# Optimization experiments

Hardware: AMD Instinct MI355X
Metric: run time of the kernel (lower is better)

## Reference

```python
import jax, jax.numpy as jnp
import numpy as np

N = 100000   # nodes
E = 1600000  # edges
G = 512      # graphs in batch
F_IN = 30
H = 128
EPS = 1e-5   # BatchNorm1d default eps


def setup_inputs() -> dict:
    key = jax.random.key(0)
    ks = jax.random.split(key, 16)
    x = jax.random.normal(ks[0], (N, F_IN), dtype=jnp.float32)
    edge_index = jax.random.randint(ks[1], (2, E), 0, N, dtype=jnp.int64)
    batch = jnp.sort(jax.random.randint(ks[2], (N,), 0, G, dtype=jnp.int64))
    d = {"x": x, "edge_index": edge_index, "batch": batch}
    dims = [(F_IN, H), (H, H), (H, H)]
    for i, (din, dout) in enumerate(dims):
        d[f"W{i}"] = jax.random.normal(ks[3 + i], (din, dout), dtype=jnp.float32) * (1.0 / np.sqrt(din))
        d[f"b{i}"] = jnp.zeros((dout,), dtype=jnp.float32)
        d[f"g{i}"] = jnp.ones((dout,), dtype=jnp.float32)   # BN gamma
        d[f"bt{i}"] = jnp.zeros((dout,), dtype=jnp.float32)  # BN beta
    d["HW1"] = jax.random.normal(ks[9], (H, 64), dtype=jnp.float32) * (1.0 / np.sqrt(H))
    d["Hb1"] = jnp.zeros((64,), dtype=jnp.float32)
    d["HW2"] = jax.random.normal(ks[10], (64, 1), dtype=jnp.float32) * 0.125
    d["Hb2"] = jnp.zeros((1,), dtype=jnp.float32)
    return d


def _bn(x, gamma, beta):
    # training-mode BatchNorm1d over node dim, biased variance (as torch uses for normalization)
    mu = jnp.mean(x, axis=0)
    var = jnp.mean(jnp.square(x - mu), axis=0)
    return (x - mu) * jax.lax.rsqrt(var + EPS) * gamma + beta


def reference(x, edge_index, batch, W0, b0, g0, bt0, W1, b1, g1, bt1, W2, b2, g2, bt2, HW1, Hb1, HW2, Hb2):
    # GCNConv: add self-loops, symmetric D^{-1/2}(A+I)D^{-1/2} normalization
    loop = jnp.arange(N, dtype=edge_index.dtype)
    src = jnp.concatenate([edge_index[0], loop])  # [E+N]
    dst = jnp.concatenate([edge_index[1], loop])
    deg = jax.ops.segment_sum(jnp.ones(src.shape, jnp.float32), dst, num_segments=N)
    dinv = jax.lax.rsqrt(jnp.maximum(deg, 1.0))  # deg >= 1 due to self-loops
    norm = (dinv[src] * dinv[dst])[:, None]      # [E+N, 1]

    for W, b, g, bt in ((W0, b0, g0, bt0), (W1, b1, g1, bt1), (W2, b2, g2, bt2)):
        h = x @ W                                           # [N, H]
        agg = jax.ops.segment_sum(h[src] * norm, dst, num_segments=N) + b
        x = jnp.maximum(_bn(agg, g, bt), 0.0)               # BN + ReLU (dropout = identity here)

    # global_mean_pool over graph ids
    counts = jax.ops.segment_sum(jnp.ones((N,), jnp.float32), batch, num_segments=G)
    pooled = jax.ops.segment_sum(x, batch, num_segments=G) / jnp.maximum(counts, 1.0)[:, None]

    h = jnp.maximum(pooled @ HW1 + Hb1, 0.0)
    return (h @ HW2 + Hb2).squeeze(-1)  # [G]
```

## Files before the change

### kernel.cpp

```cpp
#include <hip/hip_runtime.h>

#define BN_EPS 1e-5f
#define BSH 8

typedef __attribute__((ext_vector_type(8))) short bf16x8;
typedef __attribute__((ext_vector_type(4))) float f32x4;

__device__ inline float bfhi(unsigned int v) { return __uint_as_float(v & 0xFFFF0000u); }
__device__ inline float bflo(unsigned int v) { return __uint_as_float(v << 16); }
__device__ inline unsigned short f2bf(float f) {
  unsigned int u = __float_as_uint(f);
  u += 0x7FFFu + ((u >> 16) & 1u);
  return (unsigned short)(u >> 16);
}
__device__ inline unsigned int pack2bf(float lo, float hi) {
  return (unsigned int)f2bf(lo) | ((unsigned int)f2bf(hi) << 16);
}

__global__ void k_bucket(const int* __restrict__ src, const int* __restrict__ dst,
                         int* __restrict__ gcur, uint2* __restrict__ sedge,
                         int NB, int CAP, int E) {
  __shared__ int lh[512], rb[512];
  int tid = threadIdx.x;
  for (int i = tid; i < NB; i += 256) lh[i] = 0;
  __syncthreads();
  int base = blockIdx.x * 8192;
  int lim = min(8192, E - base);
  for (int i = tid; i < lim; i += 256)
    atomicAdd(&lh[dst[base + i] >> BSH], 1);
  __syncthreads();
  for (int i = tid; i < NB; i += 256) {
    int c = lh[i];
    rb[i] = c ? atomicAdd(&gcur[i], c) : 0;
    lh[i] = 0;
  }
  __syncthreads();
  for (int i = tid; i < lim; i += 256) {
    int d = dst[base + i];
    int s = src[base + i];
    int b = d >> BSH;
    int pos = rb[b] + atomicAdd(&lh[b], 1);
    if (pos < CAP) {
      uint2 v; v.x = (unsigned int)s; v.y = (unsigned int)d;
      sedge[(size_t)b * CAP + pos] = v;
    }
  }
}

__global__ void k_csr1(const uint2* __restrict__ sedge, const int* __restrict__ gcur,
                       int* __restrict__ startv, int* __restrict__ cnt,
                       float* __restrict__ dinv, int CAP, int n) {
  int b = blockIdx.x, tid = threadIdx.x;
  __shared__ int h[256], sc[256];
  h[tid] = 0;
  __syncthreads();
  int cb = gcur[b]; if (cb > CAP) cb = CAP;
  const uint2* sd = sedge + (size_t)b * CAP;
  for (int i = tid; i < cb; i += 256) atomicAdd(&h[sd[i].y & 255], 1);
  __syncthreads();
  int v = h[tid];
  sc[tid] = v;
  __syncthreads();
  for (int o = 1; o < 256; o <<= 1) {
    int t = (tid >= o) ? sc[tid - o] : 0;
    __syncthreads();
    sc[tid] += t;
    __syncthreads();
  }
  int gd = (b << BSH) + tid;
  if (gd < n) {
    startv[gd] = b * CAP + (sc[tid] - v);
    cnt[gd] = v;
    dinv[gd] = rsqrtf((float)v + 1.0f);
  }
}

__global__ void k_csr2(const uint2* __restrict__ sedge, const int* __restrict__ gcur,
                       const int* __restrict__ startv, const float* __restrict__ dinv,
                       unsigned int* __restrict__ elist, int CAP, int n) {
  int b = blockIdx.x, tid = threadIdx.x;
  __shared__ int cur[256];
  int gd = (b << BSH) + tid;
  cur[tid] = (gd < n) ? startv[gd] : 0;
  __syncthreads();
  int cb = gcur[b]; if (cb > CAP) cb = CAP;
  const uint2* sd = sedge + (size_t)b * CAP;
  for (int i = tid; i < cb; i += 256) {
    uint2 e = sd[i];
    int pos = atomicAdd(&cur[e.y & 255], 1);
    unsigned int u = (unsigned int)(dinv[e.x] * 32767.0f + 0.5f);
    elist[pos] = e.x | (u << 17);
  }
}

__global__ void k_cvtall(const float* __restrict__ x, const float* __restrict__ W0,
                         const float* __restrict__ W1, const float* __restrict__ W2,
                         unsigned short* __restrict__ xb, unsigned short* __restrict__ Wt0,
                         unsigned short* __restrict__ Wt1, unsigned short* __restrict__ Wt2,
                         int n) {
  int t = blockIdx.x * blockDim.x + threadIdx.x;
  if (t < 4096) {
    int nn = t >> 5, k = t & 31;
    Wt0[t] = f2bf(k < 30 ? W0[k * 128 + nn] : 0.f);
  } else if (t < 20480) {
    int i = t - 4096; int nn = i >> 7, k = i & 127;
    Wt1[i] = f2bf(W1[k * 128 + nn]);
  } else if (t < 36864) {
    int i = t - 20480; int nn = i >> 7, k = i & 127;
    Wt2[i] = f2bf(W2[k * 128 + nn]);
  } else {
    int i = t - 36864;
    if (i < n * 32) {
      int row = i >> 5, c = i & 31;
      xb[i] = f2bf(c < 30 ? x[row * 30 + c] : 0.f);
    }
  }
}

__global__ void k_gemm_mfma(const unsigned short* __restrict__ A,
                            const unsigned short* __restrict__ Wt,
                            const float* __restrict__ scsh, int doBN,
                            unsigned short* __restrict__ C, int n, int Kp) {
  __shared__ float ssc[128], ssh[128];
  if (doBN) {
    if (threadIdx.x < 128) {
      ssc[threadIdx.x] = scsh[threadIdx.x];
      ssh[threadIdx.x] = scsh[128 + threadIdx.x];
    }
    __syncthreads();
  }
  int wave = threadIdx.x >> 6;
  int lane = threadIdx.x & 63;
  int m0 = blockIdx.x * 128 + wave * 32;
  if (m0 >= n) return;
  int lm = lane & 15;
  int lq = lane >> 4;

  f32x4 acc[2][8] = {};
  const unsigned short* Arow0 = A + (size_t)(m0 + lm) * Kp + lq * 8;
  const unsigned short* Arow1 = Arow0 + (size_t)16 * Kp;
  const unsigned short* Bbase = Wt + (size_t)lm * Kp + lq * 8;

  for (int k0 = 0; k0 < Kp; k0 += 32) {
    uint4 ra0 = *(const uint4*)(Arow0 + k0);
    uint4 ra1 = *(const uint4*)(Arow1 + k0);
    bf16x8 a0, a1;
    if (doBN) {
      int cb = k0 + lq * 8;
      unsigned int w0 = pack2bf(fmaxf(fmaf(bflo(ra0.x), ssc[cb+0], ssh[cb+0]), 0.f),
                                fmaxf(fmaf(bfhi(ra0.x), ssc[cb+1], ssh[cb+1]), 0.f));
      unsigned int w1 = pack2bf(fmaxf(fmaf(bflo(ra0.y), ssc[cb+2], ssh[cb+2]), 0.f),
                                fmaxf(fmaf(bfhi(ra0.y), ssc[cb+3], ssh[cb+3]), 0.f));
      unsigned int w2 = pack2bf(fmaxf(fmaf(bflo(ra0.z), ssc[cb+4], ssh[cb+4]), 0.f),
                                fmaxf(fmaf(bfhi(ra0.z), ssc[cb+5], ssh[cb+5]), 0.f));
      unsigned int w3 = pack2bf(fmaxf(fmaf(bflo(ra0.w), ssc[cb+6], ssh[cb+6]), 0.f),
                                fmaxf(fmaf(bfhi(ra0.w), ssc[cb+7], ssh[cb+7]), 0.f));
      uint4 pa0 = make_uint4(w0, w1, w2, w3);
      a0 = *(bf16x8*)&pa0;
      unsigned int y0 = pack2bf(fmaxf(fmaf(bflo(ra1.x), ssc[cb+0], ssh[cb+0]), 0.f),
                                fmaxf(fmaf(bfhi(ra1.x), ssc[cb+1], ssh[cb+1]), 0.f));
      unsigned int y1 = pack2bf(fmaxf(fmaf(bflo(ra1.y), ssc[cb+2], ssh[cb+2]), 0.f),
                                fmaxf(fmaf(bfhi(ra1.y), ssc[cb+3], ssh[cb+3]), 0.f));
      unsigned int y2 = pack2bf(fmaxf(fmaf(bflo(ra1.z), ssc[cb+4], ssh[cb+4]), 0.f),
                                fmaxf(fmaf(bfhi(ra1.z), ssc[cb+5], ssh[cb+5]), 0.f));
      unsigned int y3 = pack2bf(fmaxf(fmaf(bflo(ra1.w), ssc[cb+6], ssh[cb+6]), 0.f),
                                fmaxf(fmaf(bfhi(ra1.w), ssc[cb+7], ssh[cb+7]), 0.f));
      uint4 pa1 = make_uint4(y0, y1, y2, y3);
      a1 = *(bf16x8*)&pa1;
    } else {
      a0 = *(bf16x8*)&ra0;
      a1 = *(bf16x8*)&ra1;
    }
#pragma unroll
    for (int t = 0; t < 8; ++t) {
      bf16x8 b = *(const bf16x8*)(Bbase + (size_t)t * 16 * Kp + k0);
      acc[0][t] = __builtin_amdgcn_mfma_f32_16x16x32_bf16(a0, b, acc[0][t], 0, 0, 0);
      acc[1][t] = __builtin_amdgcn_mfma_f32_16x16x32_bf16(a1, b, acc[1][t], 0, 0, 0);
    }
  }
#pragma unroll
  for (int h = 0; h < 2; ++h) {
    int rbase = m0 + h * 16 + lq * 4;
#pragma unroll
    for (int t = 0; t < 8; ++t) {
      int col = t * 16 + lm;
#pragma unroll
      for (int r = 0; r < 4; ++r) {
        int row = rbase + r;
        if (row < n) C[(size_t)row * 128 + col] = f2bf(acc[h][t][r]);
      }
    }
  }
}

__global__ void k_gather(const unsigned int* __restrict__ elist, const int* __restrict__ start,
                         const int* __restrict__ cnt, const float* __restrict__ dinv,
                         const uint4* __restrict__ h4,
                         const float* __restrict__ bias, unsigned int* __restrict__ agg,
                         float* __restrict__ bnsumP, int n) {
  int lane = threadIdx.x & 63;
  int wv   = threadIdx.x >> 6;
  int grp  = lane >> 4;
  int c8   = lane & 15;
  int row  = blockIdx.x * 4 + wv;
  bool active = row < n;

  float acc[8];
  float di = 0.f, dq = 0.f;
  int len = 0;
  const unsigned int* ep = elist;

  if (active) {
    di = dinv[row];
    dq = di * (1.0f / 32767.0f);
    len = cnt[row];
    ep = elist + start[row];
  }

  {
    float selfw = (grp == 0 && active) ? di * di : 0.f;
    float4 b0 = make_float4(0.f, 0.f, 0.f, 0.f), b1 = b0;
    if (grp == 0 && active) {
      b0 = ((const float4*)bias)[c8 * 2];
      b1 = ((const float4*)bias)[c8 * 2 + 1];
    }
    uint4 hv = active ? h4[(size_t)row * 16 + c8] : make_uint4(0, 0, 0, 0);
    acc[0] = fmaf(bflo(hv.x), selfw, b0.x);
    acc[1] = fmaf(bfhi(hv.x), selfw, b0.y);
    acc[2] = fmaf(bflo(hv.y), selfw, b0.z);
    acc[3] = fmaf(bfhi(hv.y), selfw, b0.w);
    acc[4] = fmaf(bflo(hv.z), selfw, b1.x);
    acc[5] = fmaf(bfhi(hv.z), selfw, b1.y);
    acc[6] = fmaf(bflo(hv.w), selfw, b1.z);
    acc[7] = fmaf(bfhi(hv.w), selfw, b1.w);
  }

  int j = 0;
  for (; j + 16 <= len; j += 16) {
    unsigned int e0 = ep[j + grp];
    unsigned int e1 = ep[j + 4 + grp];
    unsigned int e2 = ep[j + 8 + grp];
    unsigned int e3 = ep[j + 12 + grp];
    uint4 v0 = h4[(size_t)(e0 & 0x1FFFFu) * 16 + c8];
    uint4 v1 = h4[(size_t)(e1 & 0x1FFFFu) * 16 + c8];
    uint4 v2 = h4[(size_t)(e2 & 0x1FFFFu) * 16 + c8];
    uint4 v3 = h4[(size_t)(e3 & 0x1FFFFu) * 16 + c8];
    float w0 = (float)(e0 >> 17) * dq;
    float w1 = (float)(e1 >> 17) * dq;
    float w2 = (float)(e2 >> 17) * dq;
    float w3 = (float)(e3 >> 17) * dq;
    acc[0] = fmaf(bflo(v0.x), w0, acc[0]); acc[1] = fmaf(bfhi(v0.x), w0, acc[1]);
    acc[2] = fmaf(bflo(v0.y), w0, acc[2]); acc[3] = fmaf(bfhi(v0.y), w0, acc[3]);
    acc[4] = fmaf(bflo(v0.z), w0, acc[4]); acc[5] = fmaf(bfhi(v0.z), w0, acc[5]);
    acc[6] = fmaf(bflo(v0.w), w0, acc[6]); acc[7] = fmaf(bfhi(v0.w), w0, acc[7]);
    acc[0] = fmaf(bflo(v1.x), w1, acc[0]); acc[1] = fmaf(bfhi(v1.x), w1, acc[1]);
    acc[2] = fmaf(bflo(v1.y), w1, acc[2]); acc[3] = fmaf(bfhi(v1.y), w1, acc[3]);
    acc[4] = fmaf(bflo(v1.z), w1, acc[4]); acc[5] = fmaf(bfhi(v1.z), w1, acc[5]);
    acc[6] = fmaf(bflo(v1.w), w1, acc[6]); acc[7] = fmaf(bfhi(v1.w), w1, acc[7]);
    acc[0] = fmaf(bflo(v2.x), w2, acc[0]); acc[1] = fmaf(bfhi(v2.x), w2, acc[1]);
    acc[2] = fmaf(bflo(v2.y), w2, acc[2]); acc[3] = fmaf(bfhi(v2.y), w2, acc[3]);
    acc[4] = fmaf(bflo(v2.z), w2, acc[4]); acc[5] = fmaf(bfhi(v2.z), w2, acc[5]);
    acc[6] = fmaf(bflo(v2.w), w2, acc[6]); acc[7] = fmaf(bfhi(v2.w), w2, acc[7]);
    acc[0] = fmaf(bflo(v3.x), w3, acc[0]); acc[1] = fmaf(bfhi(v3.x), w3, acc[1]);
    acc[2] = fmaf(bflo(v3.y), w3, acc[2]); acc[3] = fmaf(bfhi(v3.y), w3, acc[3]);
    acc[4] = fmaf(bflo(v3.z), w3, acc[4]); acc[5] = fmaf(bfhi(v3.z), w3, acc[5]);
    acc[6] = fmaf(bflo(v3.w), w3, acc[6]); acc[7] = fmaf(bfhi(v3.w), w3, acc[7]);
  }
  for (; j < len; j += 4) {
    int jj = j + grp;
    unsigned int e = (jj < len) ? ep[jj] : 0u;
    uint4 v = h4[(size_t)(e & 0x1FFFFu) * 16 + c8];
    float w = (float)(e >> 17) * dq;
    acc[0] = fmaf(bflo(v.x), w, acc[0]); acc[1] = fmaf(bfhi(v.x), w, acc[1]);
    acc[2] = fmaf(bflo(v.y), w, acc[2]); acc[3] = fmaf(bfhi(v.y), w, acc[3]);
    acc[4] = fmaf(bflo(v.z), w, acc[4]); acc[5] = fmaf(bfhi(v.z), w, acc[5]);
    acc[6] = fmaf(bflo(v.w), w, acc[6]); acc[7] = fmaf(bfhi(v.w), w, acc[7]);
  }

#pragma unroll
  for (int k = 0; k < 8; ++k) {
    acc[k] += __shfl_xor(acc[k], 16);
    acc[k] += __shfl_xor(acc[k], 32);
  }

  __shared__ float sm[2][4][128];
  if (lane < 16) {
    if (active) {
      uint4 o;
      o.x = pack2bf(acc[0], acc[1]);
      o.y = pack2bf(acc[2], acc[3]);
      o.z = pack2bf(acc[4], acc[5]);
      o.w = pack2bf(acc[6], acc[7]);
      ((uint4*)agg)[(size_t)row * 16 + c8] = o;
    }
#pragma unroll
    for (int k = 0; k < 8; ++k) {
      float a = acc[k];
      sm[0][wv][c8 * 8 + k] = a;
      sm[1][wv][c8 * 8 + k] = a * a;
    }
  }
  __syncthreads();
  int tid = threadIdx.x;
  int slab = (blockIdx.x & 63) * 256;
  if (tid < 128) {
    float s = sm[0][0][tid] + sm[0][1][tid] + sm[0][2][tid] + sm[0][3][tid];
    atomicAdd(&bnsumP[slab + tid], s);
  } else {
    int c = tid - 128;
    float s = sm[1][0][c] + sm[1][1][c] + sm[1][2][c] + sm[1][3][c];
    atomicAdd(&bnsumP[slab + 128 + c], s);
  }
}

__global__ void k_bnfinal(const float* __restrict__ bnsumP, const float* __restrict__ gamma,
                          const float* __restrict__ beta, float* __restrict__ scsh, int n) {
  int c = threadIdx.x;
  float s = 0.f, s2 = 0.f;
  for (int k = 0; k < 64; ++k) {
    s  += bnsumP[k * 256 + c];
    s2 += bnsumP[k * 256 + 128 + c];
  }
  float invn = 1.0f / (float)n;
  float mu  = s * invn;
  float ex2 = s2 * invn;
  float var = fmaxf(ex2 - mu * mu, 0.f);
  float sc = gamma[c] * rsqrtf(var + BN_EPS);
  scsh[c] = sc;
  scsh[128 + c] = fmaf(-mu, sc, beta[c]);
}

__global__ void k_poolhead(const unsigned int* __restrict__ aggd, const float* __restrict__ scsh,
                           const int* __restrict__ batch, const float* __restrict__ HW1,
                           const float* __restrict__ Hb1, const float* __restrict__ HW2,
                           const float* __restrict__ Hb2, float* __restrict__ out, int n) {
  int g = blockIdx.x, t = threadIdx.x;
  int lo = 0, hi = n;
  while (lo < hi) { int mid = (lo + hi) >> 1; if (batch[mid] < g) lo = mid + 1; else hi = mid; }
  int s = lo;
  lo = 0; hi = n;
  int g1 = g + 1;
  while (lo < hi) { int mid = (lo + hi) >> 1; if (batch[mid] < g1) lo = mid + 1; else hi = mid; }
  int e = lo;

  float sc0 = scsh[2 * t], sc1 = scsh[2 * t + 1];
  float sh0 = scsh[128 + 2 * t], sh1 = scsh[128 + 2 * t + 1];
  float a0 = 0.f, a1 = 0.f;
  for (int i = s; i < e; ++i) {
    unsigned int u = aggd[(size_t)i * 64 + t];
    a0 += fmaxf(fmaf(bflo(u), sc0, sh0), 0.f);
    a1 += fmaxf(fmaf(bfhi(u), sc1, sh1), 0.f);
  }
  float inv = 1.0f / fmaxf((float)(e - s), 1.f);
  __shared__ float p[128];
  p[2 * t] = a0 * inv;
  p[2 * t + 1] = a1 * inv;
  __syncthreads();
  float acc = Hb1[t];
  for (int k = 0; k < 128; ++k) acc = fmaf(p[k], HW1[k * 64 + t], acc);
  float v = fmaxf(acc, 0.f) * HW2[t];
  for (int off = 32; off > 0; off >>= 1) v += __shfl_down(v, off);
  if (t == 0) out[g] = v + Hb2[0];
}

extern "C" void kernel_launch(void* const* d_in, const int* in_sizes, int n_in,
                              void* d_out, int out_size, void* d_ws, size_t ws_size,
                              hipStream_t stream) {
  const int F_IN = 30, H = 128;
  const float* x   = (const float*)d_in[0];
  const int* eidx  = (const int*)d_in[1];
  const int* batch = (const int*)d_in[2];
  const int N = in_sizes[0] / F_IN;
  const int E = in_sizes[1] / 2;
  const int G = out_size;
  const int* srcp = eidx;
  const int* dstp = eidx + E;
  const float* HW1 = (const float*)d_in[15];
  const float* Hb1 = (const float*)d_in[16];
  const float* HW2 = (const float*)d_in[17];
  const float* Hb2 = (const float*)d_in[18];
  float* outp = (float*)d_out;

  const int Npad = (N + 127) & ~127;
  size_t nh = (size_t)Npad * H;
  const int NB = (N + 255) >> BSH;
  const int CAP = ((E / NB) * 3) / 2 + 128;
  const int NBpad = (NB + 63) & ~63;

  unsigned short* bufH = (unsigned short*)d_ws;
  unsigned short* xbf  = bufH + nh;
  unsigned short* bufX = xbf + nh;
  float* dinv = (float*)(bufX + nh);
  int*   cnt    = (int*)(dinv + N);
  int*   startv = cnt + N;
  int*   gcur   = startv + N;
  float* bnsumP = (float*)(gcur + NBpad);
  float* scsh   = bnsumP + 3 * 64 * 256;
  unsigned short* Wt0 = (unsigned short*)(scsh + 256);
  unsigned short* Wt1 = Wt0 + 128 * 32;
  unsigned short* Wt2 = Wt1 + 128 * 128;
  unsigned int* elist = (unsigned int*)(Wt2 + 128 * 128 + 64);
  uint2* sedge = (uint2*)bufX;

  hipMemsetAsync(gcur, 0, ((size_t)NBpad + 3 * 64 * 256) * sizeof(int), stream);

  k_bucket<<<(E + 8191) / 8192, 256, 0, stream>>>(srcp, dstp, gcur, sedge, NB, CAP, E);
  k_csr1<<<NB, 256, 0, stream>>>(sedge, gcur, startv, cnt, dinv, CAP, N);
  k_csr2<<<NB, 256, 0, stream>>>(sedge, gcur, startv, dinv, elist, CAP, N);

  k_cvtall<<<(36864 + N * 32 + 255) / 256, 256, 0, stream>>>(
      x, (const float*)d_in[3], (const float*)d_in[7], (const float*)d_in[11],
      xbf, Wt0, Wt1, Wt2, N);

  const unsigned short* Wts[3] = {Wt0, Wt1, Wt2};
  for (int l = 0; l < 3; ++l) {
    const float* b  = (const float*)d_in[4 + l * 4];
    const float* gm = (const float*)d_in[5 + l * 4];
    const float* bt = (const float*)d_in[6 + l * 4];
    int Kp = (l == 0) ? 32 : 128;
    const unsigned short* Ain = (l == 0) ? xbf : bufX;
    float* bnslab = bnsumP + (size_t)l * 64 * 256;

    k_gemm_mfma<<<Npad / 128, 256, 0, stream>>>(Ain, Wts[l], scsh, l > 0, bufH, N, Kp);
    k_gather<<<(N + 3) / 4, 256, 0, stream>>>(elist, startv, cnt, dinv,
                                              (const uint4*)bufH, b,
                                              (unsigned int*)bufX, bnslab, N);
    k_bnfinal<<<1, 128, 0, stream>>>(bnslab, gm, bt, scsh, N);
  }

  k_poolhead<<<G, 64, 0, stream>>>((const unsigned int*)bufX, scsh, batch,
                                   HW1, Hb1, HW2, Hb2, outp, N);
}
```

Baseline: 523.2 us.

## Aggregate layer-0 before the GEMM, fuse BN stats into GEMM, parallelize pooling

```diff
diff --git a/kernel.cpp b/kernel.cpp
--- a/kernel.cpp
+++ b/kernel.cpp
@@ -117,10 +117,67 @@
   }
 }
 
+__global__ void k_gather0(const unsigned int* __restrict__ elist, const int* __restrict__ start,
+                          const int* __restrict__ cnt, const float* __restrict__ dinv,
+                          const uint4* __restrict__ x4,
+                          unsigned int* __restrict__ G0, int n) {
+  int lane = threadIdx.x & 63;
+  int wv   = threadIdx.x >> 6;
+  int grp  = lane >> 2;
+  int q4   = lane & 3;
+  int row  = blockIdx.x * 4 + wv;
+  bool active = row < n;
+
+  float acc[8];
+  float di = 0.f, dq = 0.f;
+  int len = 0;
+  const unsigned int* ep = elist;
+  if (active) {
+    di = dinv[row];
+    dq = di * (1.0f / 32767.0f);
+    len = cnt[row];
+    ep = elist + start[row];
+  }
+  {
+    float selfw = (grp == 0 && active) ? di * di : 0.f;
+    uint4 hv = (grp == 0 && active) ? x4[(size_t)row * 4 + q4] : make_uint4(0, 0, 0, 0);
+    acc[0] = bflo(hv.x) * selfw; acc[1] = bfhi(hv.x) * selfw;
+    acc[2] = bflo(hv.y) * selfw; acc[3] = bfhi(hv.y) * selfw;
+    acc[4] = bflo(hv.z) * selfw; acc[5] = bfhi(hv.z) * selfw;
+    acc[6] = bflo(hv.w) * selfw; acc[7] = bfhi(hv.w) * selfw;
+  }
+  for (int j = 0; j < len; j += 16) {
+    int jj = j + grp;
+    unsigned int e = (jj < len) ? ep[jj] : 0u;
+    uint4 v = x4[(size_t)(e & 0x1FFFFu) * 4 + q4];
+    float w = (float)(e >> 17) * dq;
+    acc[0] = fmaf(bflo(v.x), w, acc[0]); acc[1] = fmaf(bfhi(v.x), w, acc[1]);
+    acc[2] = fmaf(bflo(v.y), w, acc[2]); acc[3] = fmaf(bfhi(v.y), w, acc[3]);
+    acc[4] = fmaf(bflo(v.z), w, acc[4]); acc[5] = fmaf(bfhi(v.z), w, acc[5]);
+    acc[6] = fmaf(bflo(v.w), w, acc[6]); acc[7] = fmaf(bfhi(v.w), w, acc[7]);
+  }
+#pragma unroll
+  for (int k = 0; k < 8; ++k) {
+    acc[k] += __shfl_xor(acc[k], 4);
+    acc[k] += __shfl_xor(acc[k], 8);
+    acc[k] += __shfl_xor(acc[k], 16);
+    acc[k] += __shfl_xor(acc[k], 32);
+  }
+  if (grp == 0 && active) {
+    uint4 o;
+    o.x = pack2bf(acc[0], acc[1]);
+    o.y = pack2bf(acc[2], acc[3]);
+    o.z = pack2bf(acc[4], acc[5]);
+    o.w = pack2bf(acc[6], acc[7]);
+    ((uint4*)G0)[(size_t)row * 4 + q4] = o;
+  }
+}
+
 __global__ void k_gemm_mfma(const unsigned short* __restrict__ A,
                             const unsigned short* __restrict__ Wt,
                             const float* __restrict__ scsh, int doBN,
-                            unsigned short* __restrict__ C, int n, int Kp) {
+                            const float* __restrict__ bias, float* __restrict__ bnslab,
+                            int doStats, unsigned short* __restrict__ C, int n, int Kp) {
   __shared__ float ssc[128], ssh[128];
   if (doBN) {
     if (threadIdx.x < 128) {
@@ -132,7 +189,6 @@
   int wave = threadIdx.x >> 6;
   int lane = threadIdx.x & 63;
   int m0 = blockIdx.x * 128 + wave * 32;
-  if (m0 >= n) return;
   int lm = lane & 15;
   int lq = lane >> 4;
 
@@ -178,18 +234,49 @@
       acc[1][t] = __builtin_amdgcn_mfma_f32_16x16x32_bf16(a1, b, acc[1][t], 0, 0, 0);
     }
   }
+
 #pragma unroll
   for (int h = 0; h < 2; ++h) {
     int rbase = m0 + h * 16 + lq * 4;
 #pragma unroll
     for (int t = 0; t < 8; ++t) {
       int col = t * 16 + lm;
+      float bv = doStats ? bias[col] : 0.f;
 #pragma unroll
       for (int r = 0; r < 4; ++r) {
         int row = rbase + r;
-        if (row < n) C[(size_t)row * 128 + col] = f2bf(acc[h][t][r]);
+        if (row < n) C[(size_t)row * 128 + col] = f2bf(acc[h][t][r] + bv);
       }
     }
+  }
+
+  if (doStats) {
+    __shared__ float sms[4][256];
+#pragma unroll
+    for (int t = 0; t < 8; ++t) {
+      int col = t * 16 + lm;
+      float bv = bias[col];
+      float s = 0.f, s2 = 0.f;
+#pragma unroll
+      for (int h = 0; h < 2; ++h) {
+        int rbase = m0 + h * 16 + lq * 4;
+#pragma unroll
+        for (int r = 0; r < 4; ++r) {
+          if (rbase + r < n) {
+            float v = acc[h][t][r] + bv;
+            s += v; s2 = fmaf(v, v, s2);
+          }
+        }
+      }
+      s  += __shfl_xor(s, 16);  s  += __shfl_xor(s, 32);
+      s2 += __shfl_xor(s2, 16); s2 += __shfl_xor(s2, 32);
+      if (lq == 0) { sms[wave][col] = s; sms[wave][128 + col] = s2; }
+    }
+    __syncthreads();
+    int tid = threadIdx.x;
+    int slab = (blockIdx.x & 63) * 256;
+    float tot = sms[0][tid] + sms[1][tid] + sms[2][tid] + sms[3][tid];
+    atomicAdd(&bnslab[slab + tid], tot);
   }
 }
 
@@ -236,19 +323,13 @@
   }
 
   int j = 0;
-  for (; j + 16 <= len; j += 16) {
+  for (; j + 8 <= len; j += 8) {
     unsigned int e0 = ep[j + grp];
     unsigned int e1 = ep[j + 4 + grp];
-    unsigned int e2 = ep[j + 8 + grp];
-    unsigned int e3 = ep[j + 12 + grp];
     uint4 v0 = h4[(size_t)(e0 & 0x1FFFFu) * 16 + c8];
     uint4 v1 = h4[(size_t)(e1 & 0x1FFFFu) * 16 + c8];
-    uint4 v2 = h4[(size_t)(e2 & 0x1FFFFu) * 16 + c8];
-    uint4 v3 = h4[(size_t)(e3 & 0x1FFFFu) * 16 + c8];
     float w0 = (float)(e0 >> 17) * dq;
     float w1 = (float)(e1 >> 17) * dq;
-    float w2 = (float)(e2 >> 17) * dq;
-    float w3 = (float)(e3 >> 17) * dq;
     acc[0] = fmaf(bflo(v0.x), w0, acc[0]); acc[1] = fmaf(bfhi(v0.x), w0, acc[1]);
     acc[2] = fmaf(bflo(v0.y), w0, acc[2]); acc[3] = fmaf(bfhi(v0.y), w0, acc[3]);
     acc[4] = fmaf(bflo(v0.z), w0, acc[4]); acc[5] = fmaf(bfhi(v0.z), w0, acc[5]);
@@ -257,14 +338,6 @@
     acc[2] = fmaf(bflo(v1.y), w1, acc[2]); acc[3] = fmaf(bfhi(v1.y), w1, acc[3]);
     acc[4] = fmaf(bflo(v1.z), w1, acc[4]); acc[5] = fmaf(bfhi(v1.z), w1, acc[5]);
     acc[6] = fmaf(bflo(v1.w), w1, acc[6]); acc[7] = fmaf(bfhi(v1.w), w1, acc[7]);
-    acc[0] = fmaf(bflo(v2.x), w2, acc[0]); acc[1] = fmaf(bfhi(v2.x), w2, acc[1]);
-    acc[2] = fmaf(bflo(v2.y), w2, acc[2]); acc[3] = fmaf(bfhi(v2.y), w2, acc[3]);
-    acc[4] = fmaf(bflo(v2.z), w2, acc[4]); acc[5] = fmaf(bfhi(v2.z), w2, acc[5]);
-    acc[6] = fmaf(bflo(v2.w), w2, acc[6]); acc[7] = fmaf(bfhi(v2.w), w2, acc[7]);
-    acc[0] = fmaf(bflo(v3.x), w3, acc[0]); acc[1] = fmaf(bfhi(v3.x), w3, acc[1]);
-    acc[2] = fmaf(bflo(v3.y), w3, acc[2]); acc[3] = fmaf(bfhi(v3.y), w3, acc[3]);
-    acc[4] = fmaf(bflo(v3.z), w3, acc[4]); acc[5] = fmaf(bfhi(v3.z), w3, acc[5]);
-    acc[6] = fmaf(bflo(v3.w), w3, acc[6]); acc[7] = fmaf(bfhi(v3.w), w3, acc[7]);
   }
   for (; j < len; j += 4) {
     int jj = j + grp;
@@ -334,7 +407,8 @@
                            const int* __restrict__ batch, const float* __restrict__ HW1,
                            const float* __restrict__ Hb1, const float* __restrict__ HW2,
                            const float* __restrict__ Hb2, float* __restrict__ out, int n) {
-  int g = blockIdx.x, t = threadIdx.x;
+  int g = blockIdx.x;
+  int wv = threadIdx.x >> 6, t = threadIdx.x & 63;
   int lo = 0, hi = n;
   while (lo < hi) { int mid = (lo + hi) >> 1; if (batch[mid] < g) lo = mid + 1; else hi = mid; }
   int s = lo;
@@ -346,21 +420,27 @@
   float sc0 = scsh[2 * t], sc1 = scsh[2 * t + 1];
   float sh0 = scsh[128 + 2 * t], sh1 = scsh[128 + 2 * t + 1];
   float a0 = 0.f, a1 = 0.f;
-  for (int i = s; i < e; ++i) {
+  for (int i = s + wv; i < e; i += 4) {
     unsigned int u = aggd[(size_t)i * 64 + t];
     a0 += fmaxf(fmaf(bflo(u), sc0, sh0), 0.f);
     a1 += fmaxf(fmaf(bfhi(u), sc1, sh1), 0.f);
   }
-  float inv = 1.0f / fmaxf((float)(e - s), 1.f);
-  __shared__ float p[128];
-  p[2 * t] = a0 * inv;
-  p[2 * t + 1] = a1 * inv;
-  __syncthreads();
-  float acc = Hb1[t];
-  for (int k = 0; k < 128; ++k) acc = fmaf(p[k], HW1[k * 64 + t], acc);
-  float v = fmaxf(acc, 0.f) * HW2[t];
-  for (int off = 32; off > 0; off >>= 1) v += __shfl_down(v, off);
-  if (t == 0) out[g] = v + Hb2[0];
+  __shared__ float pp[4][128];
+  pp[wv][2 * t] = a0;
+  pp[wv][2 * t + 1] = a1;
+  __syncthreads();
+  if (wv == 0) {
+    float inv = 1.0f / fmaxf((float)(e - s), 1.f);
+    float p0 = (pp[0][2 * t] + pp[1][2 * t] + pp[2][2 * t] + pp[3][2 * t]) * inv;
+    float p1 = (pp[0][2 * t + 1] + pp[1][2 * t + 1] + pp[2][2 * t + 1] + pp[3][2 * t + 1]) * inv;
+    pp[0][2 * t] = p0;
+    pp[0][2 * t + 1] = p1;
+    float acc = Hb1[t];
+    for (int k = 0; k < 128; ++k) acc = fmaf(pp[0][k], HW1[k * 64 + t], acc);
+    float v = fmaxf(acc, 0.f) * HW2[t];
+    for (int off = 32; off > 0; off >>= 1) v += __shfl_down(v, off);
+    if (t == 0) out[g] = v + Hb2[0];
+  }
 }
 
 extern "C" void kernel_launch(void* const* d_in, const int* in_sizes, int n_in,
@@ -388,9 +468,10 @@
   const int NBpad = (NB + 63) & ~63;
 
   unsigned short* bufH = (unsigned short*)d_ws;
-  unsigned short* xbf  = bufH + nh;
-  unsigned short* bufX = xbf + nh;
-  float* dinv = (float*)(bufX + nh);
+  unsigned short* bufX = bufH + nh;
+  unsigned short* xbf  = bufX + nh;
+  unsigned short* G0   = xbf + (size_t)Npad * 32;
+  float* dinv = (float*)(G0 + (size_t)Npad * 32);
   int*   cnt    = (int*)(dinv + N);
   int*   startv = cnt + N;
   int*   gcur   = startv + N;
@@ -412,22 +493,31 @@
       x, (const float*)d_in[3], (const float*)d_in[7], (const float*)d_in[11],
       xbf, Wt0, Wt1, Wt2, N);
 
-  const unsigned short* Wts[3] = {Wt0, Wt1, Wt2};
-  for (int l = 0; l < 3; ++l) {
+  const float* b0  = (const float*)d_in[4];
+  const float* gm0 = (const float*)d_in[5];
+  const float* bt0 = (const float*)d_in[6];
+
+  k_gather0<<<(N + 3) / 4, 256, 0, stream>>>(elist, startv, cnt, dinv,
+                                             (const uint4*)xbf, (unsigned int*)G0, N);
+  k_gemm_mfma<<<Npad / 128, 256, 0, stream>>>(G0, Wt0, scsh, 0, b0, bnsumP, 1,
+                                              bufX, N, 32);
+  k_bnfinal<<<1, 128, 0, stream>>>(bnsumP, gm0, bt0, scsh, N);
+
+  const unsigned short* Wts[3] = {nullptr, Wt1, Wt2};
+  for (int l = 1; l < 3; ++l) {
     const float* b  = (const float*)d_in[4 + l * 4];
     const float* gm = (const float*)d_in[5 + l * 4];
     const float* bt = (const float*)d_in[6 + l * 4];
-    int Kp = (l == 0) ? 32 : 128;
-    const unsigned short* Ain = (l == 0) ? xbf : bufX;
     float* bnslab = bnsumP + (size_t)l * 64 * 256;
 
-    k_gemm_mfma<<<Npad / 128, 256, 0, stream>>>(Ain, Wts[l], scsh, l > 0, bufH, N, Kp);
+    k_gemm_mfma<<<Npad / 128, 256, 0, stream>>>(bufX, Wts[l], scsh, 1, nullptr, nullptr, 0,
+                                                bufH, N, 128);
     k_gather<<<(N + 3) / 4, 256, 0, stream>>>(elist, startv, cnt, dinv,
                                               (const uint4*)bufH, b,
                                               (unsigned int*)bufX, bnslab, N);
     k_bnfinal<<<1, 128, 0, stream>>>(bnslab, gm, bt, scsh, N);
   }
 
-  k_poolhead<<<G, 64, 0, stream>>>((const unsigned int*)bufX, scsh, batch,
-                                   HW1, Hb1, HW2, Hb2, outp, N);
-}
+  k_poolhead<<<G, 256, 0, stream>>>((const unsigned int*)bufX, scsh, batch,
+                                    HW1, Hb1, HW2, Hb2, outp, N);
+}
```

After: 461.6 us. 1.13x faster.
